# Optimization experiments

Measured on AMD Instinct MI355X. Metric: run time of the kernel, lower is better.

## Reference

```python
import jax, jax.numpy as jnp
import numpy as np

SEQ_LEN = 2048
NUM_FILTERS = 24
INPUT_DIM = 256
OUTPUT_DIM = 256
BATCH = 2
N_FFT = 4096  # nearest power of two >= 2*SEQ_LEN - 1


def _spectral_filters(L, k):
    # Hankel matrix Z_{ij} = 2 / ((i+j)^3 - (i+j)), top-k eigvecs scaled by sigma^{1/4}
    e = np.arange(1, L + 1, dtype=np.float64)
    ipj = e[:, None] + e[None, :]
    Z = 2.0 / (ipj ** 3 - ipj)
    sigma, vecs = np.linalg.eigh(Z)
    phi = vecs[:, -k:] * (sigma[-k:] ** 0.25)
    return jnp.asarray(phi, dtype=jnp.float32)


def setup_inputs() -> dict:
    key = jax.random.key(0)
    k1, k2, k3 = jax.random.split(key, 3)
    scale = (NUM_FILTERS * INPUT_DIM) ** (-0.5)
    return {
        "x": jax.random.normal(k1, (BATCH, SEQ_LEN, INPUT_DIM), jnp.float32),
        "phi": _spectral_filters(SEQ_LEN, NUM_FILTERS),  # [L, K]
        "M_phi_plus": jax.random.normal(k2, (NUM_FILTERS, INPUT_DIM, OUTPUT_DIM), jnp.float32) * scale,
        "M_phi_minus": jax.random.normal(k3, (NUM_FILTERS, INPUT_DIM, OUTPUT_DIM), jnp.float32) * scale,
    }


def _convolve(x, phi, n):
    # Faithful port of flash-stu convolve() with use_approx=False.
    B, L, I = x.shape
    K = phi.shape[1]
    # alternating sign (+1, -1, +1, ...) along the sequence
    sgn = jnp.where(jnp.arange(L) % 2 == 0, 1.0, -1.0).astype(x.dtype)[None, :, None, None]  # (1,L,1,1)
    v = jnp.fft.rfft(phi, n=n, axis=0)[None, :, :, None, None]  # (1, n//2+1, K, 1, 1)
    u = jnp.broadcast_to(x[:, :, None, :, None], (B, L, K, I, 1))  # (B,L,K,I,1)
    U = jnp.concatenate([u, u * sgn[..., None]], axis=-1)          # (B,L,K,I,2)
    U_f = jnp.fft.rfft(U, n=n, axis=1)                             # (B,n//2+1,K,I,2)
    U_conv = jnp.fft.irfft(v * U_f, n=n, axis=1)[:, :L]            # (B,L,K,I,2)
    U_plus = U_conv[..., 0]
    U_minus = U_conv[..., 1] * sgn                                 # (B,L,K,I)
    return U_plus, U_minus


def reference(x, phi, M_phi_plus, M_phi_minus):
    U_plus, U_minus = _convolve(x, phi, N_FFT)
    spectral_plus = jnp.einsum('blki,kio->blo', U_plus, M_phi_plus)
    spectral_minus = jnp.einsum('blki,kio->blo', U_minus, M_phi_minus)
    return spectral_plus + spectral_minus
```

## Files before the change

kernel.cpp:

```cpp
#include <hip/hip_runtime.h>
#include <hip/hip_bf16.h>

#define SL 2048
#define NK 24
#define NI 256
#define NO 256
#define NB 2
#define NC 48
#define TD 64

typedef __bf16 bf16x8 __attribute__((ext_vector_type(8)));
typedef float f32x4 __attribute__((ext_vector_type(4)));
typedef unsigned short u16x8 __attribute__((ext_vector_type(8)));
typedef unsigned short ushort_t;
typedef unsigned int u32;

#define OFF_G   0ull
#define SZ_G    (8ull*48*2304*2)
#define OFF_MT  (OFF_G + 14155776ull)
#define SZ_MT   (48ull*256*256*2)
#define OFF_XB  (OFF_MT + SZ_MT)
#define SZ_XB   (2ull*2048*256*2)
#define OFF_YT  (OFF_XB + SZ_XB)
#define SZ_YT   (2ull*48*256*2048*2)
#define WS_NEED (OFF_YT + SZ_YT)

__device__ __forceinline__ unsigned short f2bf(float f) {
    unsigned int u = __float_as_uint(f);
    unsigned int r = (u + 0x7FFFu + ((u >> 16) & 1u)) >> 16;
    return (unsigned short)r;
}

__device__ __forceinline__ void glds16(ushort_t* l, const ushort_t* g) {
    __builtin_amdgcn_global_load_lds((const __attribute__((address_space(1))) u32*)g,
                                     (__attribute__((address_space(3))) u32*)l, 16, 0, 0);
}

__global__ __launch_bounds__(256) void k_prep(const float* __restrict__ x,
                                              const float* __restrict__ phi,
                                              const float* __restrict__ Mp,
                                              const float* __restrict__ Mm,
                                              ushort_t* __restrict__ xb,
                                              ushort_t* __restrict__ mt,
                                              ushort_t* __restrict__ G) {
    __shared__ float tile[64][65];
    int blk = blockIdx.x, tid = threadIdx.x;
    if (blk < 1024) {
        int i = blk * 256 + tid;
        float4 v = reinterpret_cast<const float4*>(x)[i];
        ushort4 o;
        o.x = f2bf(v.x); o.y = f2bf(v.y); o.z = f2bf(v.z); o.w = f2bf(v.w);
        reinterpret_cast<ushort4*>(xb)[i] = o;
    } else if (blk < 1792) {
        int id = blk - 1024;
        int c = id >> 4, it = (id >> 2) & 3, ot = id & 3;
        int k = c >> 1;
        const float* M = (c & 1) ? Mm : Mp;
        int col = tid & 63, rq = tid >> 6;
        for (int rr = 0; rr < 64; rr += 4) {
            int i = rr + rq;
            tile[i][col] = M[((k * NI) + (it * 64 + i)) * NO + ot * 64 + col];
        }
        __syncthreads();
        for (int rr = 0; rr < 64; rr += 4) {
            int o = rr + rq;
            mt[((c * NO) + (ot * 64 + o)) * NI + it * 64 + col] = f2bf(tile[col][o]);
        }
    } else {
        int id = blk - 1792;
        int p = id / 48, c = id - p * 48;
        int k = c >> 1, odd = c & 1;
        ushort_t* Gpc = G + (size_t)(p * 48 + c) * 2304;
#pragma unroll
        for (int i = 0; i < 9; ++i) {
            int j = i * 256 + tid;
            int s = 2047 - (j + p);
            float v = 0.f;
            if (s >= 0 && s < SL) {
                v = phi[s * NK + k];
                if (odd && (s & 1)) v = -v;
            }
            Gpc[j] = f2bf(v);
        }
    }
}

__global__ __launch_bounds__(256, 4) void k_gemm1(const ushort_t* __restrict__ XB,
                                                  const ushort_t* __restrict__ MT,
                                                  ushort_t* __restrict__ yt) {
    __shared__ ushort_t sh[17408];
    int nb_ = blockIdx.x;
    int rb  = blockIdx.y;
    int n0 = nb_ * 128;
    int tid = threadIdx.x, lane = tid & 63, wid = tid >> 6;
    int wr = wid >> 1, wc = wid & 1;
    int ln15 = lane & 15, lq = lane >> 4;
    int swz = lq ^ ((ln15 >> 1) & 3);

    const ushort_t* Arow = XB + (size_t)(rb * 128) * 256;
    const ushort_t* Brow = MT + (size_t)n0 * 256;

    auto stage = [&](int bufsel, int s) {
        ushort_t* L = sh + bufsel * 8192;
        int k0 = s * 32;
#pragma unroll
        for (int jj = 0; jj < 2; ++jj) {
            int flat = tid + jj * 256;
            int row = flat >> 2;
            int k8s = (flat & 3) ^ ((flat >> 3) & 3);
            glds16(L + flat * 8, Arow + row * 256 + k0 + k8s * 8);
        }
#pragma unroll
        for (int jj = 0; jj < 2; ++jj) {
            int flat = tid + jj * 256;
            int row = flat >> 2;
            int k8s = (flat & 3) ^ ((flat >> 3) & 3);
            glds16(L + 4096 + flat * 8, Brow + row * 256 + k0 + k8s * 8);
        }
    };

    f32x4 acc[4][4];
    f32x4 z = {0.f, 0.f, 0.f, 0.f};
#pragma unroll
    for (int mi = 0; mi < 4; ++mi)
#pragma unroll
        for (int ni = 0; ni < 4; ++ni) acc[mi][ni] = z;

    stage(0, 0);
    __syncthreads();
    for (int s = 0; s < 8; ++s) {
        int cur = s & 1;
        if (s < 7) stage(cur ^ 1, s + 1);
        const ushort_t* Ab = sh + cur * 8192;
        const ushort_t* Bb = Ab + 4096;
        bf16x8 af[4], bfr[4];
#pragma unroll
        for (int mi = 0; mi < 4; ++mi)
            af[mi] = *reinterpret_cast<const bf16x8*>(Ab + (wr * 64 + mi * 16 + ln15) * 32 + swz * 8);
#pragma unroll
        for (int ni = 0; ni < 4; ++ni)
            bfr[ni] = *reinterpret_cast<const bf16x8*>(Bb + (wc * 64 + ni * 16 + ln15) * 32 + swz * 8);
#pragma unroll
        for (int mi = 0; mi < 4; ++mi)
#pragma unroll
            for (int ni = 0; ni < 4; ++ni)
                acc[mi][ni] = __builtin_amdgcn_mfma_f32_16x16x32_bf16(af[mi], bfr[ni], acc[mi][ni], 0, 0, 0);
        __syncthreads();
    }

    ushort_t* OT = sh;
#pragma unroll
    for (int mi = 0; mi < 4; ++mi)
#pragma unroll
        for (int ni = 0; ni < 4; ++ni) {
            int t_loc = wr * 64 + mi * 16 + lq * 4;
            int n_loc = wc * 64 + ni * 16 + ln15;
            ushort4 pk;
            pk.x = f2bf(acc[mi][ni][0]);
            pk.y = f2bf(acc[mi][ni][1]);
            pk.z = f2bf(acc[mi][ni][2]);
            pk.w = f2bf(acc[mi][ni][3]);
            *reinterpret_cast<ushort4*>(OT + n_loc * 136 + t_loc) = pk;
        }
    __syncthreads();
    int b = rb >> 4;
    int tt0 = (rb & 15) * 2;
#pragma unroll
    for (int jj = 0; jj < 8; ++jj) {
        int flat = tid + jj * 256;
        int n_loc = flat >> 4, te = (flat & 15) * 8;
        int nn = n0 + n_loc;
        int c = nn >> 8, o = nn & 255;
        int tt = tt0 + (te >> 6), tp = te & 63;
        *reinterpret_cast<u16x8*>(yt + ((((size_t)(b * NC + c) * 32 + tt) << 8) + o) * 64 + tp) =
            *reinterpret_cast<const u16x8*>(OT + n_loc * 136 + te);
    }
}

#define LOAD_SET(SA, SB, SLOT, AB, BB) do {                                        \
    _Pragma("unroll") for (int m = 0; m < 8; ++m)                                  \
        SA[m] = *(const bf16x8*)((AB) + aBase + (SLOT) + m * 2048);                \
    _Pragma("unroll") for (int n2 = 0; n2 < 4; ++n2)                               \
        SB[n2] = *(const bf16x8*)((BB) + bBase + (SLOT) + n2 * 2048);              \
} while (0)

#define MFMA_SET(SA, SB) do {                                                      \
    _Pragma("unroll") for (int m = 0; m < 8; ++m)                                  \
    _Pragma("unroll") for (int n2 = 0; n2 < 4; ++n2)                               \
        acc[m][n2] = __builtin_amdgcn_mfma_f32_16x16x32_bf16(                      \
            SA[m], SB[n2], acc[m][n2], 0, 0, 0);                                   \
} while (0)

__global__ __launch_bounds__(512, 2) void k_conv8(const ushort_t* __restrict__ Gb,
                                                  const ushort_t* __restrict__ yt,
                                                  float* __restrict__ out) {
    __shared__ ushort_t sh[65536];

    int blk = blockIdx.x;
    int orig = (blk & 7) * 32 + (blk >> 3);
    const int NBt[8] = {4, 7, 11, 14, 18, 21, 25, 28};
    int b_ = orig >> 7;
    int j = orig & 127;
    int pp = 0, base = 0;
    while (pp < 7 && j >= base + NBt[pp]) { base += NBt[pp]; ++pp; }
    int idx = j - base, n = NBt[pp];
    int U = 192 * (pp + 1);
    int u0 = idx * U / n, u1 = (idx + 1) * U / n;

    int tid = threadIdx.x, lane = tid & 63, wid = tid >> 6;
    int wr = wid >> 2, wc = wid & 3;
    int ln15 = lane & 15, lq = lane >> 4;

    const ushort_t* YTb = yt + (size_t)b_ * NC * 32 * 16384;
    const char* shc = (const char*)sh;

    int s0l = (lq ^ (ln15 & 7)) * 16;
    int s1l = ((4 + lq) ^ (ln15 & 7)) * 16;
    int aBase = (wr * 128 + ln15) * 128;
    int bBase = (wc * 64 + ln15) * 128;
    int w2  = wid >> 2;
    int dAl = tid * 8;
    int dBl = w2 * 4096 + (wid & 3) * 512 + lane * 8;
    int gB2 = (((tid >> 3) & 31) + w2 * 64) * 64 + ((tid & 7) ^ ((tid >> 3) & 7)) * 8;
    int srow = tid >> 3;
    int ti0 = ((tid & 7) ^ (srow & 7)) * 8;
    int rho = (7 - srow) & 7;
    int aG0 = rho * 48 * 2304 + 2239 - srow + ti0 - rho;

    auto stageA = [&](ushort_t* L, int tt, int c) {
        int aGc = aG0 + c * 2304 - 64 * (4 * pp - tt + 3);
#pragma unroll
        for (int jj = 0; jj < 2; ++jj)
#pragma unroll
            for (int qm = 0; qm < 2; ++qm)
                glds16(L + jj * 8192 + qm * 4096 + dAl,
                       Gb + aGc - 64 * (jj * 2 + qm));
    };
    auto stageB = [&](ushort_t* L, int tt, int c) {
        const ushort_t* Ub = YTb + (((size_t)(c * 32 + tt)) << 14) + gB2;
#pragma unroll
        for (int jj = 0; jj < 2; ++jj)
#pragma unroll
            for (int qn = 0; qn < 2; ++qn)
                glds16(L + jj * 8192 + qn * 2048 + dBl,
                       Ub + jj * 8192 + qn * 2048);
    };
    auto stageU = [&](int u) {
        int tt = u / 48, c = u - tt * 48;
        stageA(sh + ((u & 1) << 14), tt, c);
        stageB(sh + 32768 + ((u & 1) << 14), tt, c);
    };

    f32x4 acc[8][4];
    f32x4 z = {0.f, 0.f, 0.f, 0.f};
#pragma unroll
    for (int mi = 0; mi < 8; ++mi)
#pragma unroll
        for (int ni = 0; ni < 4; ++ni) acc[mi][ni] = z;

    bf16x8 s0a[8], s0b[4], s1a[8], s1b[4];

    stageU(u0);
    stageU(u0 + 1);
    asm volatile("s_waitcnt vmcnt(8)" ::: "memory");
    asm volatile("s_barrier" ::: "memory");
    {
        const char* AB = shc + ((u0 & 1) << 15);
        const char* BB = shc + 65536 + ((u0 & 1) << 15);
        LOAD_SET(s0a, s0b, s0l, AB, BB);
    }

    for (int s = u0; s < u1; ++s) {
        const char* AB = shc + ((s & 1) << 15);
        const char* BB = shc + 65536 + ((s & 1) << 15);

        LOAD_SET(s1a, s1b, s1l, AB, BB);
        __builtin_amdgcn_sched_barrier(0);

        __builtin_amdgcn_s_setprio(1);
        MFMA_SET(s0a, s0b);
        __builtin_amdgcn_s_setprio(0);

        asm volatile("s_waitcnt lgkmcnt(0)" ::: "memory");
        asm volatile("s_waitcnt vmcnt(0)" ::: "memory");
        __builtin_amdgcn_sched_barrier(0);
        asm volatile("s_barrier" ::: "memory");

        if (s + 2 < u1) stageU(s + 2);

        if (s + 1 < u1) {
            const char* AB2 = shc + (((s + 1) & 1) << 15);
            const char* BB2 = shc + 65536 + (((s + 1) & 1) << 15);
            LOAD_SET(s0a, s0b, s0l, AB2, BB2);
        }
        __builtin_amdgcn_sched_barrier(0);

        __builtin_amdgcn_s_setprio(1);
        MFMA_SET(s1a, s1b);
        __builtin_amdgcn_s_setprio(0);
        __builtin_amdgcn_sched_barrier(0);
    }

    float* outp = out + (((size_t)b_ * SL) + (size_t)pp * 256) * NO;
#pragma unroll
    for (int mi = 0; mi < 8; ++mi)
#pragma unroll
        for (int ni = 0; ni < 4; ++ni) {
            int l = wr * 128 + mi * 16 + lq * 4;
            int o = wc * 64 + ni * 16 + ln15;
#pragma unroll
            for (int r = 0; r < 4; ++r)
                atomicAdd(&outp[(size_t)(l + r) * NO + o], acc[mi][ni][r]);
        }
}

extern "C" void kernel_launch(void* const* d_in, const int* in_sizes, int n_in,
                              void* d_out, int out_size, void* d_ws, size_t ws_size,
                              hipStream_t stream) {
    const float* x   = (const float*)d_in[0];
    const float* phi = (const float*)d_in[1];
    const float* Mp  = (const float*)d_in[2];
    const float* Mm  = (const float*)d_in[3];
    float* out = (float*)d_out;

    if (ws_size < WS_NEED) return;

    char* ws = (char*)d_ws;
    ushort_t* G  = (ushort_t*)(ws + OFF_G);
    ushort_t* MT = (ushort_t*)(ws + OFF_MT);
    ushort_t* XB = (ushort_t*)(ws + OFF_XB);
    ushort_t* YT = (ushort_t*)(ws + OFF_YT);

    hipMemsetAsync(d_out, 0, (size_t)out_size * sizeof(float), stream);
    k_prep<<<dim3(2176), dim3(256), 0, stream>>>(x, phi, Mp, Mm, XB, MT, G);
    k_gemm1<<<dim3(96, 32), dim3(256), 0, stream>>>(XB, MT, YT);
    k_conv8<<<dim3(256), dim3(512), 0, stream>>>(G, YT, out);
}
```

Measured before the change: 178.4 us.

## Load Toeplitz A-operand directly from global into registers, drop its LDS staging

The A operand (filter Toeplitz matrix) is no longer staged through shared memory. Each lane now reads its bf16x8 fragments straight from global memory, using a per-lane base pointer that follows the diagonal Toeplitz structure, while only the B operand stays double-buffered in LDS. This halves LDS use and removes the A-side async copies and LDS reads. The cost is global-load latency in the MFMA loop, which relies on cache hits, and the vmcnt waits are changed to match.

```diff
diff --git a/kernel.cpp b/kernel.cpp
--- a/kernel.cpp
+++ b/kernel.cpp
@@ -177,9 +177,10 @@
     }
 }
 
-#define LOAD_SET(SA, SB, SLOT, AB, BB) do {                                        \
+#define LOAD_SET(SA, SB, SLOT, KK, BB, TT, CC) do {                                \
+    const ushort_t* Ga_ = Gl + (CC) * 2304 + (TT) * 64 + (KK) * 32;                \
     _Pragma("unroll") for (int m = 0; m < 8; ++m)                                  \
-        SA[m] = *(const bf16x8*)((AB) + aBase + (SLOT) + m * 2048);                \
+        SA[m] = *(const bf16x8*)(Ga_ - m * 16);                                    \
     _Pragma("unroll") for (int n2 = 0; n2 < 4; ++n2)                               \
         SB[n2] = *(const bf16x8*)((BB) + bBase + (SLOT) + n2 * 2048);              \
 } while (0)
@@ -194,7 +195,7 @@
 __global__ __launch_bounds__(512, 2) void k_conv8(const ushort_t* __restrict__ Gb,
                                                   const ushort_t* __restrict__ yt,
                                                   float* __restrict__ out) {
-    __shared__ ushort_t sh[65536];
+    __shared__ ushort_t sh[32768];
 
     int blk = blockIdx.x;
     int orig = (blk & 7) * 32 + (blk >> 3);
@@ -216,26 +217,13 @@
 
     int s0l = (lq ^ (ln15 & 7)) * 16;
     int s1l = ((4 + lq) ^ (ln15 & 7)) * 16;
-    int aBase = (wr * 128 + ln15) * 128;
     int bBase = (wc * 64 + ln15) * 128;
     int w2  = wid >> 2;
-    int dAl = tid * 8;
     int dBl = w2 * 4096 + (wid & 3) * 512 + lane * 8;
     int gB2 = (((tid >> 3) & 31) + w2 * 64) * 64 + ((tid & 7) ^ ((tid >> 3) & 7)) * 8;
-    int srow = tid >> 3;
-    int ti0 = ((tid & 7) ^ (srow & 7)) * 8;
-    int rho = (7 - srow) & 7;
-    int aG0 = rho * 48 * 2304 + 2239 - srow + ti0 - rho;
-
-    auto stageA = [&](ushort_t* L, int tt, int c) {
-        int aGc = aG0 + c * 2304 - 64 * (4 * pp - tt + 3);
-#pragma unroll
-        for (int jj = 0; jj < 2; ++jj)
-#pragma unroll
-            for (int qm = 0; qm < 2; ++qm)
-                glds16(L + jj * 8192 + qm * 4096 + dAl,
-                       Gb + aGc - 64 * (jj * 2 + qm));
-    };
+    int pA = (7 - ln15) & 7;
+    const ushort_t* Gl = Gb + pA * 110592 + 2047 - pA - ln15 - wr * 128 - pp * 256 + lq * 8;
+
     auto stageB = [&](ushort_t* L, int tt, int c) {
         const ushort_t* Ub = YTb + (((size_t)(c * 32 + tt)) << 14) + gB2;
 #pragma unroll
@@ -245,11 +233,6 @@
                 glds16(L + jj * 8192 + qn * 2048 + dBl,
                        Ub + jj * 8192 + qn * 2048);
     };
-    auto stageU = [&](int u) {
-        int tt = u / 48, c = u - tt * 48;
-        stageA(sh + ((u & 1) << 14), tt, c);
-        stageB(sh + 32768 + ((u & 1) << 14), tt, c);
-    };
 
     f32x4 acc[8][4];
     f32x4 z = {0.f, 0.f, 0.f, 0.f};
@@ -258,23 +241,28 @@
 #pragma unroll
         for (int ni = 0; ni < 4; ++ni) acc[mi][ni] = z;
 
+    int tc = u0 / 48, cc = u0 - tc * 48;
+    int t1 = tc, c1 = cc;
+    if (++c1 == 48) { c1 = 0; ++t1; }
+    int t2 = t1, c2 = c1;
+    if (++c2 == 48) { c2 = 0; ++t2; }
+
     bf16x8 s0a[8], s0b[4], s1a[8], s1b[4];
 
-    stageU(u0);
-    stageU(u0 + 1);
-    asm volatile("s_waitcnt vmcnt(8)" ::: "memory");
+    stageB(sh + ((u0 & 1) << 14), tc, cc);
+    stageB(sh + (((u0 + 1) & 1) << 14), t1, c1);
+    asm volatile("s_waitcnt vmcnt(4)" ::: "memory");
     asm volatile("s_barrier" ::: "memory");
     {
-        const char* AB = shc + ((u0 & 1) << 15);
-        const char* BB = shc + 65536 + ((u0 & 1) << 15);
-        LOAD_SET(s0a, s0b, s0l, AB, BB);
+        const char* BB0 = shc + ((u0 & 1) << 15);
+        LOAD_SET(s0a, s0b, s0l, 0, BB0, tc, cc);
     }
 
     for (int s = u0; s < u1; ++s) {
-        const char* AB = shc + ((s & 1) << 15);
-        const char* BB = shc + 65536 + ((s & 1) << 15);
-
-        LOAD_SET(s1a, s1b, s1l, AB, BB);
+        const char* BBc = shc + ((s & 1) << 15);
+        const char* BBn = shc + (((s + 1) & 1) << 15);
+
+        LOAD_SET(s1a, s1b, s1l, 1, BBc, tc, cc);
         __builtin_amdgcn_sched_barrier(0);
 
         __builtin_amdgcn_s_setprio(1);
@@ -282,16 +270,14 @@
         __builtin_amdgcn_s_setprio(0);
 
         asm volatile("s_waitcnt lgkmcnt(0)" ::: "memory");
-        asm volatile("s_waitcnt vmcnt(0)" ::: "memory");
+        asm volatile("s_waitcnt vmcnt(8)" ::: "memory");
         __builtin_amdgcn_sched_barrier(0);
         asm volatile("s_barrier" ::: "memory");
 
-        if (s + 2 < u1) stageU(s + 2);
+        if (s + 2 < u1) stageB(sh + ((s & 1) << 14), t2, c2);
 
         if (s + 1 < u1) {
-            const char* AB2 = shc + (((s + 1) & 1) << 15);
-            const char* BB2 = shc + 65536 + (((s + 1) & 1) << 15);
-            LOAD_SET(s0a, s0b, s0l, AB2, BB2);
+            LOAD_SET(s0a, s0b, s0l, 0, BBn, t1, c1);
         }
         __builtin_amdgcn_sched_barrier(0);
 
@@ -299,6 +285,9 @@
         MFMA_SET(s1a, s1b);
         __builtin_amdgcn_s_setprio(0);
         __builtin_amdgcn_sched_barrier(0);
+
+        tc = t1; cc = c1; t1 = t2; c1 = c2;
+        if (++c2 == 48) { c2 = 0; ++t2; }
     }
 
     float* outp = out + (((size_t)b_ * SL) + (size_t)pp * 256) * NO;
```

New measurement: 325.9 us. +82.7%, slower.
